# Kernel tuning notes

Measured on AMD Instinct MI355X. Metric: run time of the kernel, lower is better.

## Reference

```python
import jax, jax.numpy as jnp
import numpy as np

B, N, C, H = 8192, 36, 128, 8
HD = C // H  # 16
FOCUS = 3
EPS = 1e-4


def setup_inputs() -> dict:
    key = jax.random.key(0)
    ks = jax.random.split(key, 10)
    x = jax.random.normal(ks[0], (B, N, C), dtype=jnp.float32)
    pos = jax.random.normal(ks[1], (B, N, C), dtype=jnp.float32)
    mask = jax.random.randint(ks[2], (B, N), 0, 2).astype(jnp.float32)
    coords = jax.random.randint(ks[3], (B * N, 4), 0, 8).astype(jnp.int64)
    voxel_inds = jax.random.permutation(ks[4], B * N).reshape(B, N).astype(jnp.int64)
    s = 0.02
    qk_w = jax.random.normal(ks[5], (C, 2 * C), dtype=jnp.float32) * s
    qk_b = jnp.zeros((2 * C,), dtype=jnp.float32)
    v_w = jax.random.normal(ks[6], (C, C), dtype=jnp.float32) * s
    v_b = jnp.zeros((C,), dtype=jnp.float32)
    proj_w = jax.random.normal(ks[7], (C, C), dtype=jnp.float32) * s
    proj_b = jnp.zeros((C,), dtype=jnp.float32)
    return {"x": x, "pos": pos, "mask": mask, "qk_w": qk_w, "qk_b": qk_b,
            "v_w": v_w, "v_b": v_b, "proj_w": proj_w, "proj_b": proj_b,
            "coords": coords, "voxel_inds": voxel_inds}


def reference(x, pos, mask, qk_w, qk_b, v_w, v_b, proj_w, proj_b, coords, voxel_inds):
    b, n, c = x.shape
    qk = (x + pos) @ qk_w + qk_b                      # (B,N,2C)
    q, k = qk[..., :c], qk[..., c:]
    v = x @ v_w + v_b                                 # (B,N,C)
    k = k * mask[..., None]
    # split heads -> (B,H,N,HD)
    q = q.reshape(b, n, H, HD).transpose(0, 2, 1, 3)
    k = k.reshape(b, n, H, HD).transpose(0, 2, 1, 3)
    v = v.reshape(b, n, H, HD).transpose(0, 2, 1, 3)
    # focusing power
    q = q ** FOCUS
    k = k ** FOCUS
    # q normalized per-token over channels; k normalized per-channel over tokens
    # (original rearranges k to (bh, c, n) before norm(dim=-1))
    q = q / (EPS + jnp.linalg.norm(q, axis=-1, keepdims=True))
    k = k / (EPS + jnp.linalg.norm(k, axis=2, keepdims=True))
    # linear attention: kv = k^T v (HD x HD), then q @ kv
    kv = jnp.einsum('bhnc,bhnd->bhcd', k, v)          # (B,H,HD,HD)
    out = jnp.einsum('bhnc,bhcd->bhnd', q, kv)        # (B,H,N,HD)
    out = out.transpose(0, 2, 1, 3).reshape(b, n, c)  # (B,N,C)
    num = jnp.sum(mask, axis=-1, keepdims=True)       # (B,1)
    out = out / (num[..., None] + EPS)
    # inverse-permutation gather: perm[voxel_inds.flat] = arange
    flat = voxel_inds.reshape(-1)
    M = coords.shape[0]
    perm = jnp.zeros((M,), dtype=flat.dtype).at[flat].set(
        jnp.arange(M, dtype=flat.dtype))
    out = out.reshape(-1, c)[perm]                    # (M,C)
    out = out @ proj_w + proj_b
    return out
```

## Files before the change

### kernel.cpp

```cpp
#include <hip/hip_runtime.h>

typedef __bf16 bf16x8 __attribute__((ext_vector_type(8)));
typedef float f32x4 __attribute__((ext_vector_type(4)));

#define Bdim 8192
#define Nn 36
#define Cc 128
#define EPSf 1e-4f

#define WS_QK_HI 0
#define WS_QK_LO 32768
#define WS_V_HI  65536
#define WS_P_HI  81920

#define OFF_XH   0
#define OFF_PH   12288
#define OFF_PL   24576
#define OFF_KT   0
#define OFF_VT   14336
#define OFF_KV   28672
#define OFF_QH   38912
#define OFF_O    0
#define OFF_MASK 51200
#define OFF_VOX  51392
#define OFF_INN  51584
#define LDS_BYTES 51712

__device__ inline uint bfh(float f) {
    __bf16 h = (__bf16)f;
    return (uint)(*(const ushort*)&h);
}
__device__ inline uint bfl(float f) {
    float hf = (float)((__bf16)f);
    __bf16 l = (__bf16)(f - hf);
    return (uint)(*(const ushort*)&l);
}
__device__ inline uint pk2h(float a, float b) { return bfh(a) | (bfh(b) << 16); }
__device__ inline uint pk2l(float a, float b) { return bfl(a) | (bfl(b) << 16); }

union U8 { bf16x8 v; uint u[4]; };

__global__ __launch_bounds__(256)
void prep_frags(const float* __restrict__ qk_w, const float* __restrict__ v_w,
                const float* __restrict__ proj_w, ushort* __restrict__ ws)
{
    int e = blockIdx.x * 256 + threadIdx.x;
    const float* W; int N; int idx; int hi_off; int lo_off;
    if (e < 32768)      { W = qk_w;   N = 256; hi_off = WS_QK_HI; lo_off = WS_QK_LO; idx = e; }
    else if (e < 49152) { W = v_w;    N = 128; hi_off = WS_V_HI;  lo_off = -1;       idx = e - 32768; }
    else                { W = proj_w; N = 128; hi_off = WS_P_HI;  lo_off = -1;       idx = e - 49152; }
    int j    = idx & 7;
    int lane = (idx >> 3) & 63;
    int ks   = (idx >> 9) & 3;
    int ct   = idx >> 11;
    int col  = ct * 16 + (lane & 15);
    int k    = ks * 32 + (lane >> 4) * 8 + j;
    float v  = W[k * N + col];
    ws[hi_off + idx] = (ushort)bfh(v);
    if (lo_off >= 0) ws[lo_off + idx] = (ushort)bfl(v);
}

__global__ __launch_bounds__(512, 6)
void fla_mfma(const float* __restrict__ x, const float* __restrict__ pos,
              const float* __restrict__ mask, const float* __restrict__ qk_b,
              const float* __restrict__ v_b, const float* __restrict__ proj_b,
              const int* __restrict__ vox, const ushort* __restrict__ ws,
              float* __restrict__ out)
{
    __shared__ __align__(16) char lds[LDS_BYTES];
    const int t = threadIdx.x;
    const int b = blockIdx.x;
    const int lane = t & 63;
    const int wv = t >> 6;

    const uint sw   = ((uint)lane & 7u) << 4;
    const int  rsel = lane & 15;
    const int  grp  = lane >> 4;
    const uint kgrp = (uint)grp * 8u;

    const float* xg = x + (size_t)b * (Nn * Cc);
    const float* pg = pos + (size_t)b * (Nn * Cc);
    #pragma unroll
    for (int it = 0; it < 3; ++it) {
        int idx = t + it * 512;
        int n = idx >> 5;
        int c4 = (idx & 31) << 2;
        float4 xv = make_float4(0.f, 0.f, 0.f, 0.f);
        float4 pv = make_float4(0.f, 0.f, 0.f, 0.f);
        if (n < Nn) {
            xv = *(const float4*)(xg + n * Cc + c4);
            pv = *(const float4*)(pg + n * Cc + c4);
        }
        float s0 = xv.x + pv.x, s1 = xv.y + pv.y, s2 = xv.z + pv.z, s3 = xv.w + pv.w;
        uint ba = (uint)n * 256u + (((uint)(c4 * 2)) ^ (((uint)n & 7u) << 4));
        *(uint2*)(lds + OFF_XH + ba) = make_uint2(pk2h(xv.x, xv.y), pk2h(xv.z, xv.w));
        *(uint2*)(lds + OFF_PH + ba) = make_uint2(pk2h(s0, s1), pk2h(s2, s3));
        *(uint2*)(lds + OFF_PL + ba) = make_uint2(pk2l(s0, s1), pk2l(s2, s3));
    }
    if (t < 48) ((float*)(lds + OFF_MASK))[t] = (t < Nn) ? mask[(size_t)b * Nn + t] : 0.f;
    if (t >= 64 && t < 64 + Nn) ((int*)(lds + OFF_VOX))[t - 64] = vox[(size_t)b * Nn + (t - 64)];
    if (t == 128) {
        float s = 0.f;
        for (int n = 0; n < Nn; ++n) s += mask[(size_t)b * Nn + n];
        *(float*)(lds + OFF_INN) = 1.f / (s + EPSf);
    }
    __syncthreads();

    f32x4 accV[3];
    f32x4 accQ[3][2];
    #pragma unroll
    for (int rt = 0; rt < 3; ++rt) {
        accV[rt] = (f32x4){0.f, 0.f, 0.f, 0.f};
        accQ[rt][0] = (f32x4){0.f, 0.f, 0.f, 0.f};
        accQ[rt][1] = (f32x4){0.f, 0.f, 0.f, 0.f};
    }
    #pragma unroll
    for (int ks = 0; ks < 4; ++ks) {
        uint ka = (((uint)(ks * 32) + kgrp) * 2u) ^ sw;
        bf16x8 xh[3];
        #pragma unroll
        for (int rt = 0; rt < 3; ++rt)
            xh[rt] = *(const bf16x8*)(lds + OFF_XH + (uint)(rt * 16 + rsel) * 256u + ka);
        int f = ((wv * 4 + ks) * 64 + lane) * 8;
        bf16x8 bvh = *(const bf16x8*)(ws + WS_V_HI + f);
        #pragma unroll
        for (int rt = 0; rt < 3; ++rt)
            accV[rt] = __builtin_amdgcn_mfma_f32_16x16x32_bf16(xh[rt], bvh, accV[rt], 0, 0, 0);
    }
    #pragma unroll
    for (int ks = 0; ks < 4; ++ks) {
        uint ka = (((uint)(ks * 32) + kgrp) * 2u) ^ sw;
        bf16x8 ph[3], pl[3];
        #pragma unroll
        for (int rt = 0; rt < 3; ++rt) {
            uint ba = (uint)(rt * 16 + rsel) * 256u + ka;
            ph[rt] = *(const bf16x8*)(lds + OFF_PH + ba);
            pl[rt] = *(const bf16x8*)(lds + OFF_PL + ba);
        }
        #pragma unroll
        for (int ci = 0; ci < 2; ++ci) {
            int f = (((wv * 2 + ci) * 4 + ks) * 64 + lane) * 8;
            bf16x8 bh = *(const bf16x8*)(ws + WS_QK_HI + f);
            bf16x8 bl = *(const bf16x8*)(ws + WS_QK_LO + f);
            #pragma unroll
            for (int rt = 0; rt < 3; ++rt) {
                accQ[rt][ci] = __builtin_amdgcn_mfma_f32_16x16x32_bf16(ph[rt], bh, accQ[rt][ci], 0, 0, 0);
                accQ[rt][ci] = __builtin_amdgcn_mfma_f32_16x16x32_bf16(ph[rt], bl, accQ[rt][ci], 0, 0, 0);
                accQ[rt][ci] = __builtin_amdgcn_mfma_f32_16x16x32_bf16(pl[rt], bh, accQ[rt][ci], 0, 0, 0);
            }
        }
    }
    __syncthreads();

    const float* sM = (const float*)(lds + OFF_MASK);
    {
        int colv = wv * 16 + rsel;
        float vb = v_b[colv];
        #pragma unroll
        for (int rt = 0; rt < 3; ++rt) {
            float a0 = accV[rt][0] + vb, a1 = accV[rt][1] + vb;
            float a2 = accV[rt][2] + vb, a3 = accV[rt][3] + vb;
            uint addr = OFF_VT + (uint)(colv * 56 + rt * 16 + grp * 4) * 2u;
            *(uint2*)(lds + addr) = make_uint2(pk2h(a0, a1), pk2h(a2, a3));
        }
    }
    if (wv < 4) {
        #pragma unroll
        for (int ci = 0; ci < 2; ++ci) {
            int colq = (wv * 2 + ci) * 16 + rsel;
            float qb = qk_b[colq];
            uint cb2 = (uint)(colq * 2);
            #pragma unroll
            for (int rt = 0; rt < 3; ++rt) {
                #pragma unroll
                for (int r = 0; r < 4; ++r) {
                    int row = rt * 16 + grp * 4 + r;
                    float q1 = accQ[rt][ci][r] + qb;
                    float q3 = q1 * q1 * q1;
                    uint ba = (uint)row * 256u + (cb2 ^ (((uint)row & 7u) << 4));
                    *(ushort*)(lds + OFF_QH + ba) = (ushort)bfh(q3);
                }
            }
        }
    } else {
        #pragma unroll
        for (int ci = 0; ci < 2; ++ci) {
            int colk = ((wv - 4) * 2 + ci) * 16 + rsel;
            float kb = qk_b[Cc + colk];
            #pragma unroll
            for (int rt = 0; rt < 3; ++rt) {
                float k3v[4];
                #pragma unroll
                for (int r = 0; r < 4; ++r) {
                    int row = rt * 16 + grp * 4 + r;
                    float k1 = (accQ[rt][ci][r] + kb) * sM[row];
                    k3v[r] = k1 * k1 * k1;
                }
                uint addr = OFF_KT + (uint)(colk * 56 + rt * 16 + grp * 4) * 2u;
                *(uint2*)(lds + addr) = make_uint2(pk2h(k3v[0], k3v[1]), pk2h(k3v[2], k3v[3]));
            }
        }
    }
    __syncthreads();

    {
        int c16 = rsel;
        int col16 = wv * 16 + c16;
        uint a0 = OFF_KT + (uint)(col16 * 56 + grp * 8) * 2u;
        uint b0 = OFF_VT + (uint)(col16 * 56 + grp * 8) * 2u;
        bf16x8 kA0 = *(const bf16x8*)(lds + a0);
        bf16x8 vB0 = *(const bf16x8*)(lds + b0);
        U8 kA1, vB1;
        kA1.u[0] = kA1.u[1] = kA1.u[2] = kA1.u[3] = 0u;
        vB1.u[0] = vB1.u[1] = vB1.u[2] = vB1.u[3] = 0u;
        if (grp < 2) {
            kA1.v = *(const bf16x8*)(lds + a0 + 64);
            vB1.v = *(const bf16x8*)(lds + b0 + 64);
        }
        float s = 0.f;
        #pragma unroll
        for (int j = 0; j < 8; ++j) { float q = (float)kA0[j]; s += q * q; }
        #pragma unroll
        for (int j = 0; j < 8; ++j) { float q = (float)kA1.v[j]; s += q * q; }
        s += __shfl_xor(s, 16);
        s += __shfl_xor(s, 32);
        float invkn = 1.f / (EPSf + sqrtf(s));

        f32x4 kvacc = (f32x4){0.f, 0.f, 0.f, 0.f};
        kvacc = __builtin_amdgcn_mfma_f32_16x16x32_bf16(kA0, vB0, kvacc, 0, 0, 0);
        kvacc = __builtin_amdgcn_mfma_f32_16x16x32_bf16(kA1.v, vB1.v, kvacc, 0, 0, 0);

        float* kvp = (float*)(lds + OFF_KV) + wv * 320;
        #pragma unroll
        for (int r = 0; r < 4; ++r) {
            int c_out = grp * 4 + r;
            float fac = __shfl(invkn, c_out);
            kvp[c_out * 20 + c16] = kvacc[r] * fac;
        }
    }
    __syncthreads();

    {
        int d = rsel;
        float inn = *(const float*)(lds + OFF_INN);
        U8 bkv;
        bkv.u[0] = bkv.u[1] = bkv.u[2] = bkv.u[3] = 0u;
        if (grp < 2) {
            const float* kvp = (const float*)(lds + OFF_KV) + wv * 320 + (grp * 8) * 20 + d;
            float f0 = kvp[0],  f1 = kvp[20], f2 = kvp[40],  f3 = kvp[60];
            float f4 = kvp[80], f5 = kvp[100], f6 = kvp[120], f7 = kvp[140];
            bkv.u[0] = pk2h(f0, f1); bkv.u[1] = pk2h(f2, f3);
            bkv.u[2] = pk2h(f4, f5); bkv.u[3] = pk2h(f6, f7);
        }
        f32x4 oacc[3];
        float invn[3];
        #pragma unroll
        for (int rt = 0; rt < 3; ++rt) {
            int row = rt * 16 + rsel;
            U8 aq;
            aq.u[0] = aq.u[1] = aq.u[2] = aq.u[3] = 0u;
            if (grp < 2) {
                uint ba = (uint)row * 256u +
                          (((uint)((wv * 16 + grp * 8) * 2)) ^ (((uint)row & 7u) << 4));
                aq.v = *(const bf16x8*)(lds + OFF_QH + ba);
            }
            float s = 0.f;
            #pragma unroll
            for (int j = 0; j < 8; ++j) { float q = (float)aq.v[j]; s += q * q; }
            s += __shfl_xor(s, 16);
            invn[rt] = 1.f / (EPSf + sqrtf(s));
            f32x4 o = (f32x4){0.f, 0.f, 0.f, 0.f};
            o = __builtin_amdgcn_mfma_f32_16x16x32_bf16(aq.v, bkv.v, o, 0, 0, 0);
            oacc[rt] = o;
        }
        #pragma unroll
        for (int rt = 0; rt < 3; ++rt) {
            #pragma unroll
            for (int r = 0; r < 4; ++r) {
                int rr = grp * 4 + r;
                int row = rt * 16 + rr;
                float fac = __shfl(invn[rt], rr) * inn;
                float val = oacc[rt][r] * fac;
                uint ba = (uint)row * 256u +
                          (((uint)((wv * 16 + d) * 2)) ^ (((uint)row & 7u) << 4));
                *(ushort*)(lds + OFF_O + ba) = (ushort)bfh(val);
            }
        }
    }
    __syncthreads();

    f32x4 accP[3];
    #pragma unroll
    for (int rt = 0; rt < 3; ++rt) accP[rt] = (f32x4){0.f, 0.f, 0.f, 0.f};
    #pragma unroll
    for (int ks = 0; ks < 4; ++ks) {
        uint ka = (((uint)(ks * 32) + kgrp) * 2u) ^ sw;
        bf16x8 oa[3];
        #pragma unroll
        for (int rt = 0; rt < 3; ++rt)
            oa[rt] = *(const bf16x8*)(lds + OFF_O + (uint)(rt * 16 + rsel) * 256u + ka);
        int f = ((wv * 4 + ks) * 64 + lane) * 8;
        bf16x8 bp = *(const bf16x8*)(ws + WS_P_HI + f);
        #pragma unroll
        for (int rt = 0; rt < 3; ++rt)
            accP[rt] = __builtin_amdgcn_mfma_f32_16x16x32_bf16(oa[rt], bp, accP[rt], 0, 0, 0);
    }
    {
        const int* sVx = (const int*)(lds + OFF_VOX);
        int col = wv * 16 + rsel;
        float pb = proj_b[col];
        #pragma unroll
        for (int rt = 0; rt < 3; ++rt) {
            #pragma unroll
            for (int r = 0; r < 4; ++r) {
                int row = rt * 16 + grp * 4 + r;
                if (row < Nn)
                    out[(size_t)sVx[row] * Cc + col] = accP[rt][r] + pb;
            }
        }
    }
}

extern "C" void kernel_launch(void* const* d_in, const int* in_sizes, int n_in,
                              void* d_out, int out_size, void* d_ws, size_t ws_size,
                              hipStream_t stream) {
    (void)in_sizes; (void)n_in; (void)out_size; (void)ws_size;
    const float* x      = (const float*)d_in[0];
    const float* pos    = (const float*)d_in[1];
    const float* mask   = (const float*)d_in[2];
    const float* qk_w   = (const float*)d_in[3];
    const float* qk_b   = (const float*)d_in[4];
    const float* v_w    = (const float*)d_in[5];
    const float* v_b    = (const float*)d_in[6];
    const float* proj_w = (const float*)d_in[7];
    const float* proj_b = (const float*)d_in[8];
    const int*   vox    = (const int*)d_in[10];
    ushort* ws = (ushort*)d_ws;
    float* outp = (float*)d_out;

    hipLaunchKernelGGL(prep_frags, dim3(256), dim3(256), 0, stream, qk_w, v_w, proj_w, ws);
    hipLaunchKernelGGL(fla_mfma, dim3(Bdim), dim3(512), 0, stream,
                       x, pos, mask, qk_b, v_b, proj_b, vox, ws, outp);
}
```

Measured before the change: 222.3 us.

## Shrink LDS footprint, widen swizzle, store kv as packed bf16 for occupancy

Reorganizes the LDS layout: K/V transposed tiles use a tighter 48-element stride, the Q buffer only holds the 36 valid rows, and the kv matrix is stored pre-packed as bf16 in a layout read back with one 16-byte load instead of eight strided float reads. This cuts LDS per block from about 51.7KB to about 40.4KB, and the launch-bounds occupancy hint goes from 6 to 8. The XOR swizzle is widened from 8 to 16 row phases to reduce bank conflicts. Risks include new bank conflicts from the 48-element stride and register pressure under the higher occupancy target.

```diff
diff --git a/kernel.cpp b/kernel.cpp
--- a/kernel.cpp
+++ b/kernel.cpp
@@ -17,14 +17,14 @@
 #define OFF_PH   12288
 #define OFF_PL   24576
 #define OFF_KT   0
-#define OFF_VT   14336
-#define OFF_KV   28672
-#define OFF_QH   38912
+#define OFF_VT   12288
+#define OFF_QH   24576
+#define OFF_KV   33792
 #define OFF_O    0
-#define OFF_MASK 51200
-#define OFF_VOX  51392
-#define OFF_INN  51584
-#define LDS_BYTES 51712
+#define OFF_MASK 39936
+#define OFF_VOX  40128
+#define OFF_INN  40272
+#define LDS_BYTES 40448
 
 __device__ inline uint bfh(float f) {
     __bf16 h = (__bf16)f;
@@ -60,7 +60,7 @@
     if (lo_off >= 0) ws[lo_off + idx] = (ushort)bfl(v);
 }
 
-__global__ __launch_bounds__(512, 6)
+__global__ __launch_bounds__(512, 8)
 void fla_mfma(const float* __restrict__ x, const float* __restrict__ pos,
               const float* __restrict__ mask, const float* __restrict__ qk_b,
               const float* __restrict__ v_b, const float* __restrict__ proj_b,
@@ -73,10 +73,10 @@
     const int lane = t & 63;
     const int wv = t >> 6;
 
-    const uint sw   = ((uint)lane & 7u) << 4;
     const int  rsel = lane & 15;
     const int  grp  = lane >> 4;
     const uint kgrp = (uint)grp * 8u;
+    const uint sw   = ((uint)rsel) << 4;
 
     const float* xg = x + (size_t)b * (Nn * Cc);
     const float* pg = pos + (size_t)b * (Nn * Cc);
@@ -92,7 +92,7 @@
             pv = *(const float4*)(pg + n * Cc + c4);
         }
         float s0 = xv.x + pv.x, s1 = xv.y + pv.y, s2 = xv.z + pv.z, s3 = xv.w + pv.w;
-        uint ba = (uint)n * 256u + (((uint)(c4 * 2)) ^ (((uint)n & 7u) << 4));
+        uint ba = (uint)n * 256u + (((uint)(c4 * 2)) ^ (((uint)n & 15u) << 4));
         *(uint2*)(lds + OFF_XH + ba) = make_uint2(pk2h(xv.x, xv.y), pk2h(xv.z, xv.w));
         *(uint2*)(lds + OFF_PH + ba) = make_uint2(pk2h(s0, s1), pk2h(s2, s3));
         *(uint2*)(lds + OFF_PL + ba) = make_uint2(pk2l(s0, s1), pk2l(s2, s3));
@@ -160,7 +160,7 @@
         for (int rt = 0; rt < 3; ++rt) {
             float a0 = accV[rt][0] + vb, a1 = accV[rt][1] + vb;
             float a2 = accV[rt][2] + vb, a3 = accV[rt][3] + vb;
-            uint addr = OFF_VT + (uint)(colv * 56 + rt * 16 + grp * 4) * 2u;
+            uint addr = OFF_VT + (uint)(colv * 48 + rt * 16 + grp * 4) * 2u;
             *(uint2*)(lds + addr) = make_uint2(pk2h(a0, a1), pk2h(a2, a3));
         }
     }
@@ -175,10 +175,12 @@
                 #pragma unroll
                 for (int r = 0; r < 4; ++r) {
                     int row = rt * 16 + grp * 4 + r;
-                    float q1 = accQ[rt][ci][r] + qb;
-                    float q3 = q1 * q1 * q1;
-                    uint ba = (uint)row * 256u + (cb2 ^ (((uint)row & 7u) << 4));
-                    *(ushort*)(lds + OFF_QH + ba) = (ushort)bfh(q3);
+                    if (row < Nn) {
+                        float q1 = accQ[rt][ci][r] + qb;
+                        float q3 = q1 * q1 * q1;
+                        uint ba = (uint)row * 256u + (cb2 ^ (((uint)row & 15u) << 4));
+                        *(ushort*)(lds + OFF_QH + ba) = (ushort)bfh(q3);
+                    }
                 }
             }
         }
@@ -196,7 +198,7 @@
                     float k1 = (accQ[rt][ci][r] + kb) * sM[row];
                     k3v[r] = k1 * k1 * k1;
                 }
-                uint addr = OFF_KT + (uint)(colk * 56 + rt * 16 + grp * 4) * 2u;
+                uint addr = OFF_KT + (uint)(colk * 48 + rt * 16 + grp * 4) * 2u;
                 *(uint2*)(lds + addr) = make_uint2(pk2h(k3v[0], k3v[1]), pk2h(k3v[2], k3v[3]));
             }
         }
@@ -204,10 +206,9 @@
     __syncthreads();
 
     {
-        int c16 = rsel;
-        int col16 = wv * 16 + c16;
-        uint a0 = OFF_KT + (uint)(col16 * 56 + grp * 8) * 2u;
-        uint b0 = OFF_VT + (uint)(col16 * 56 + grp * 8) * 2u;
+        int col16 = wv * 16 + rsel;
+        uint a0 = OFF_KT + (uint)(col16 * 48 + grp * 8) * 2u;
+        uint b0 = OFF_VT + (uint)(col16 * 48 + grp * 8) * 2u;
         bf16x8 kA0 = *(const bf16x8*)(lds + a0);
         bf16x8 vB0 = *(const bf16x8*)(lds + b0);
         U8 kA1, vB1;
@@ -230,13 +231,13 @@
         kvacc = __builtin_amdgcn_mfma_f32_16x16x32_bf16(kA0, vB0, kvacc, 0, 0, 0);
         kvacc = __builtin_amdgcn_mfma_f32_16x16x32_bf16(kA1.v, vB1.v, kvacc, 0, 0, 0);
 
-        float* kvp = (float*)(lds + OFF_KV) + wv * 320;
-        #pragma unroll
-        for (int r = 0; r < 4; ++r) {
-            int c_out = grp * 4 + r;
-            float fac = __shfl(invkn, c_out);
-            kvp[c_out * 20 + c16] = kvacc[r] * fac;
-        }
+        float f0 = __shfl(invkn, grp * 4 + 0);
+        float f1 = __shfl(invkn, grp * 4 + 1);
+        float f2 = __shfl(invkn, grp * 4 + 2);
+        float f3 = __shfl(invkn, grp * 4 + 3);
+        uint addr = OFF_KV + (uint)(wv * 384 + rsel * 24 + grp * 4) * 2u;
+        *(uint2*)(lds + addr) =
+            make_uint2(pk2h(kvacc[0] * f0, kvacc[1] * f1), pk2h(kvacc[2] * f2, kvacc[3] * f3));
     }
     __syncthreads();
 
@@ -245,13 +246,8 @@
         float inn = *(const float*)(lds + OFF_INN);
         U8 bkv;
         bkv.u[0] = bkv.u[1] = bkv.u[2] = bkv.u[3] = 0u;
-        if (grp < 2) {
-            const float* kvp = (const float*)(lds + OFF_KV) + wv * 320 + (grp * 8) * 20 + d;
-            float f0 = kvp[0],  f1 = kvp[20], f2 = kvp[40],  f3 = kvp[60];
-            float f4 = kvp[80], f5 = kvp[100], f6 = kvp[120], f7 = kvp[140];
-            bkv.u[0] = pk2h(f0, f1); bkv.u[1] = pk2h(f2, f3);
-            bkv.u[2] = pk2h(f4, f5); bkv.u[3] = pk2h(f6, f7);
-        }
+        if (grp < 2)
+            bkv.v = *(const bf16x8*)(lds + OFF_KV + (uint)(wv * 384 + d * 24 + grp * 8) * 2u);
         f32x4 oacc[3];
         float invn[3];
         #pragma unroll
@@ -259,9 +255,9 @@
             int row = rt * 16 + rsel;
             U8 aq;
             aq.u[0] = aq.u[1] = aq.u[2] = aq.u[3] = 0u;
-            if (grp < 2) {
+            if (grp < 2 && row < Nn) {
                 uint ba = (uint)row * 256u +
-                          (((uint)((wv * 16 + grp * 8) * 2)) ^ (((uint)row & 7u) << 4));
+                          (((uint)((wv * 16 + grp * 8) * 2)) ^ (((uint)row & 15u) << 4));
                 aq.v = *(const bf16x8*)(lds + OFF_QH + ba);
             }
             float s = 0.f;
@@ -282,7 +278,7 @@
                 float fac = __shfl(invn[rt], rr) * inn;
                 float val = oacc[rt][r] * fac;
                 uint ba = (uint)row * 256u +
-                          (((uint)((wv * 16 + d) * 2)) ^ (((uint)row & 7u) << 4));
+                          (((uint)((wv * 16 + d) * 2)) ^ (((uint)row & 15u) << 4));
                 *(ushort*)(lds + OFF_O + ba) = (ushort)bfh(val);
             }
         }
```

New measurement: 234.9 us. 5.7% more time.
